# Kernel optimization log

Measured on AMD Instinct MI355X. Metric: run time of the kernel, lower is better.

The kernel has to match this reference:

```python
import jax, jax.numpy as jnp
import numpy as np

NUM_NEIGHBORS = (10, 25)  # FLAGS.num_neighbors = '10_25'
MAX_DEGREE = 64
L = 2  # num encoder layers


def _sample(nodes, neighbors_out, neighbors_in, key):
    """Multi-hop uniform neighbor sampling (shuffle columns + slice, as in TF code)."""
    samples = [nodes]
    support = 1
    supports = [1]
    for k in range(L):
        t = L - 1 - k
        n = NUM_NEIGHBORS[t]
        support *= 2 * n
        supports.append(support)
        key, k1, k2 = jax.random.split(key, 3)
        # tf.transpose(tf.random.shuffle(tf.transpose(x))) shuffles neighbor slots
        # with ONE permutation shared across all rows, then slices first n.
        cols_out = jax.random.permutation(k1, MAX_DEGREE)[:n]
        cols_in = jax.random.permutation(k2, MAX_DEGREE)[:n]
        nout = neighbors_out[samples[k]][:, cols_out]  # [prev, n]
        nin = neighbors_in[samples[k]][:, cols_in]     # [prev, n]
        samples.append(jnp.concatenate([nout, nin], axis=1).reshape(-1))
    return samples, supports


def _gc(self_v, nei_out, nei_in, W):
    # GraphConvolution: mean-aggregate out/in neighbors, concat with self, linear, sigmoid.
    agg = jnp.concatenate([self_v, nei_out.mean(axis=1), nei_in.mean(axis=1)], axis=-1)
    return jax.nn.sigmoid(agg @ W)


def _aggregate(inputs, supports, layer, W, B):
    h_hop = []
    for hop in range(L - layer):
        n = NUM_NEIGHBORS[L - hop - 1]
        nei = inputs[hop + 1].reshape(B * supports[hop], 2 * n, -1)
        self_v = inputs[hop].reshape(B * supports[hop], -1)
        h_hop.append(_gc(self_v, nei[:, :n], nei[:, n:], W))
    return h_hop


def _forward(nodes1, nodes2, neighbors_out, neighbors_in, features,
             W_in, W_mean, W_std, W_pi, W_ag, W_ad, Wd_mean, Wd_std, Wd_pi):
    B = nodes1.shape[0]
    key = jax.random.key(42)
    k1, k2 = jax.random.split(key)
    s1, sup1 = _sample(nodes1, neighbors_out, neighbors_in, k1)
    s2, sup2 = _sample(nodes2, neighbors_out, neighbors_in, k2)
    in1 = [features[s] for s in s1]  # hop-wise gathered features
    in2 = [features[s] for s in s2]
    # layer 0: shared input GC
    h1 = _aggregate(in1, sup1, 0, W_in, B)
    h2 = _aggregate(in2, sup2, 0, W_in, B)
    # layer 1: parameter heads (mean/std/pi/alpha)
    h_mean1 = _aggregate(h1, sup1, 1, W_mean, B)[0]
    h_mean2 = _aggregate(h2, sup2, 1, W_mean, B)[0]
    h_std1 = _aggregate(h1, sup1, 1, W_std, B)[0]
    h_std2 = _aggregate(h2, sup2, 1, W_std, B)[0]
    h_pi1 = _aggregate(h1, sup1, 1, W_pi, B)[0]
    h_pi2 = _aggregate(h2, sup2, 1, W_pi, B)[0]
    # final fully-connected projections (act = identity)
    z_mean1 = h_mean1 @ Wd_mean
    z_mean2 = h_mean2 @ Wd_mean
    z_std1 = h_std1 @ Wd_std
    z_std2 = h_std2 @ Wd_std
    pi_logit1 = h_pi1 @ Wd_pi
    pi_logit2 = h_pi2 @ Wd_pi
    return jnp.stack([z_mean1, z_std1, pi_logit1, z_mean2, z_std2, pi_logit2])


def setup_inputs() -> dict:
    key = jax.random.key(0)
    ks = jax.random.split(key, 16)
    N, F, B = 200000, 128, 256
    E, D = 128, 64
    inp = {
        'nodes1': jax.random.randint(ks[0], (B,), 0, N, dtype=jnp.int32),
        'nodes2': jax.random.randint(ks[1], (B,), 0, N, dtype=jnp.int32),
        'neighbors_out': jax.random.randint(ks[2], (N, MAX_DEGREE), 0, N, dtype=jnp.int32),
        'neighbors_in': jax.random.randint(ks[3], (N, MAX_DEGREE), 0, N, dtype=jnp.int32),
        'features': jax.random.normal(ks[4], (N, F), dtype=jnp.float32),
        'W_in': jax.random.normal(ks[5], (3 * F, E), dtype=jnp.float32) * 0.05,
        'W_mean': jax.random.normal(ks[6], (3 * E, E), dtype=jnp.float32) * 0.05,
        'W_std': jax.random.normal(ks[7], (3 * E, E), dtype=jnp.float32) * 0.05,
        'W_pi': jax.random.normal(ks[8], (3 * E, E), dtype=jnp.float32) * 0.05,
        'W_ag': jax.random.normal(ks[9], (3 * E, E), dtype=jnp.float32) * 0.05,
        'W_ad': jax.random.normal(ks[10], (3 * E, E), dtype=jnp.float32) * 0.05,
        'Wd_mean': jax.random.normal(ks[11], (E, D), dtype=jnp.float32) * 0.05,
        'Wd_std': jax.random.normal(ks[12], (E, D), dtype=jnp.float32) * 0.05,
        'Wd_pi': jax.random.normal(ks[13], (E, D), dtype=jnp.float32) * 0.05,
    }
    return inp


def reference(nodes1, nodes2, neighbors_out, neighbors_in, features,
              W_in, W_mean, W_std, W_pi, W_ag, W_ad, Wd_mean, Wd_std, Wd_pi):
    return _forward(nodes1, nodes2, neighbors_out, neighbors_in, features,
                    W_in, W_mean, W_std, W_pi, W_ag, W_ad, Wd_mean, Wd_std, Wd_pi)
```

## Files before the change

### kernel.cpp

```cpp
#include <hip/hip_runtime.h>
#include <stdint.h>
#include <math.h>

#define FDIM 128
#define KDIM 384
#define NROWS 26112

struct Cols { int o25[25]; int i25[25]; int o10[10]; int i10[10]; };
struct ColsBoth { Cols c[2]; };

static inline uint32_t rotl32(uint32_t x, uint32_t r){ return (x<<r)|(x>>(32u-r)); }

static void tf2x32(uint32_t k0, uint32_t k1, uint32_t c0, uint32_t c1,
                   uint32_t& o0, uint32_t& o1){
  const uint32_t ra[4] = {13u,15u,26u,6u};
  const uint32_t rb[4] = {17u,29u,16u,24u};
  uint32_t ks2 = k0 ^ k1 ^ 0x1BD11BDAu;
  uint32_t x0 = c0 + k0, x1 = c1 + k1;
  for(int i=0;i<4;i++){ x0 += x1; x1 = rotl32(x1, ra[i]); x1 ^= x0; }
  x0 += k1; x1 += ks2 + 1u;
  for(int i=0;i<4;i++){ x0 += x1; x1 = rotl32(x1, rb[i]); x1 ^= x0; }
  x0 += ks2; x1 += k0 + 2u;
  for(int i=0;i<4;i++){ x0 += x1; x1 = rotl32(x1, ra[i]); x1 ^= x0; }
  x0 += k0; x1 += k1 + 3u;
  for(int i=0;i<4;i++){ x0 += x1; x1 = rotl32(x1, rb[i]); x1 ^= x0; }
  x0 += k1; x1 += ks2 + 4u;
  for(int i=0;i<4;i++){ x0 += x1; x1 = rotl32(x1, ra[i]); x1 ^= x0; }
  x0 += ks2; x1 += k0 + 5u;
  o0 = x0; o1 = x1;
}

static void jax_split_child(uint32_t ka, uint32_t kb, uint32_t i,
                            uint32_t& oa, uint32_t& ob){
  tf2x32(ka, kb, 0u, i, oa, ob);
}

static uint32_t jax_bits32(uint32_t ka, uint32_t kb, uint32_t i){
  uint32_t a,b; tf2x32(ka, kb, 0u, i, a, b);
  return a ^ b;
}

static void jax_perm64(uint32_t ka, uint32_t kb, int* perm){
  uint32_t sa, sb; jax_split_child(ka, kb, 1u, sa, sb);
  uint32_t b[64]; int v[64];
  for(int i=0;i<64;i++){ b[i]=jax_bits32(sa, sb, (uint32_t)i); v[i]=i; }
  for(int i=1;i<64;i++){
    uint32_t bb=b[i]; int vv=v[i]; int j=i-1;
    while(j>=0 && b[j]>bb){ b[j+1]=b[j]; v[j+1]=v[j]; j--; }
    b[j+1]=bb; v[j+1]=vv;
  }
  for(int i=0;i<64;i++) perm[i]=v[i];
}

static void compute_cols(ColsBoth& cb){
  uint32_t k1a,k1b,k2a,k2b;
  jax_split_child(0u, 42u, 0u, k1a, k1b);
  jax_split_child(0u, 42u, 1u, k2a, k2b);
  for(int side=0; side<2; side++){
    uint32_t ka = side ? k2a : k1a;
    uint32_t kb = side ? k2b : k1b;
    uint32_t nka,nkb, c1a,c1b, c2a,c2b;
    jax_split_child(ka,kb,0u,nka,nkb);
    jax_split_child(ka,kb,1u,c1a,c1b);
    jax_split_child(ka,kb,2u,c2a,c2b);
    int p[64];
    jax_perm64(c1a,c1b,p); for(int i=0;i<25;i++) cb.c[side].o25[i]=p[i];
    jax_perm64(c2a,c2b,p); for(int i=0;i<25;i++) cb.c[side].i25[i]=p[i];
    uint32_t d1a,d1b,d2a,d2b;
    jax_split_child(nka,nkb,1u,d1a,d1b);
    jax_split_child(nka,nkb,2u,d2a,d2b);
    jax_perm64(d1a,d1b,p); for(int i=0;i<10;i++) cb.c[side].o10[i]=p[i];
    jax_perm64(d2a,d2b,p); for(int i=0;i<10;i++) cb.c[side].i10[i]=p[i];
  }
}

__device__ __forceinline__ float getc(const float4& v, int i){
  return (i==0)?v.x:(i==1)?v.y:(i==2)?v.z:v.w;
}
__device__ __forceinline__ float sigf(float x){ return 1.0f/(1.0f+expf(-x)); }
__device__ __forceinline__ void add4(float4& s, const float4& v){
  s.x+=v.x; s.y+=v.y; s.z+=v.z; s.w+=v.w;
}


__global__ __launch_bounds__(256) void sample1_kernel(
    const int* __restrict__ nodes1, const int* __restrict__ nodes2,
    const int* __restrict__ nout, const int* __restrict__ nin,
    int* __restrict__ s_hop1, ColsBoth cb){
  int idx = blockIdx.x*blockDim.x + threadIdx.x;
  if(idx >= 2*256*50) return;
  int side = idx / (256*50);
  int rem  = idx % (256*50);
  int b = rem / 50, j = rem % 50;
  int node = (side ? nodes2 : nodes1)[b];
  const Cols& c = cb.c[side];
  int nbr = (j < 25) ? nout[(long)node*64 + c.o25[j]]
                     : nin [(long)node*64 + c.i25[j-25]];
  s_hop1[idx] = nbr;
}

__global__ __launch_bounds__(256) void gather_kernel(
    const float* __restrict__ feat,
    const int* __restrict__ nodes1, const int* __restrict__ nodes2,
    const int* __restrict__ s_hop1,
    const int* __restrict__ nout, const int* __restrict__ nin,
    float* __restrict__ agg, int base_row, ColsBoth cb)
{
  int t = threadIdx.x;
  int row_local = blockIdx.x*8 + (t>>5);
  int lane = t & 31;
  int c0 = lane*4;
  int row = base_row + row_local;

  float4 selfv, so, si;

  if(row < 512){
    int side = row >> 8, b = row & 255;
    int node = (side ? nodes2 : nodes1)[b];
    selfv = *(const float4*)(feat + (long)node*FDIM + c0);
    const int* nb = s_hop1 + row*50;
    float4 acc = make_float4(0,0,0,0);
    #pragma unroll
    for(int jj=0; jj<25; jj+=5){
      int id[5]; float4 v[5];
      #pragma unroll
      for(int i=0;i<5;i++) id[i] = nb[jj+i];
      #pragma unroll
      for(int i=0;i<5;i++) v[i] = *(const float4*)(feat + (long)id[i]*FDIM + c0);
      #pragma unroll
      for(int i=0;i<5;i++) add4(acc, v[i]);
    }
    so = make_float4(acc.x/25.f, acc.y/25.f, acc.z/25.f, acc.w/25.f);
    acc = make_float4(0,0,0,0);
    #pragma unroll
    for(int jj=25; jj<50; jj+=5){
      int id[5]; float4 v[5];
      #pragma unroll
      for(int i=0;i<5;i++) id[i] = nb[jj+i];
      #pragma unroll
      for(int i=0;i<5;i++) v[i] = *(const float4*)(feat + (long)id[i]*FDIM + c0);
      #pragma unroll
      for(int i=0;i<5;i++) add4(acc, v[i]);
    }
    si = make_float4(acc.x/25.f, acc.y/25.f, acc.z/25.f, acc.w/25.f);
  } else {
    int hrow = row - 512;
    int side = (hrow >= 12800) ? 1 : 0;
    int node = s_hop1[hrow];
    const Cols& c = cb.c[side];
    const long nb = (long)node*64;
    int oid[10], iid[10];
    #pragma unroll
    for(int j=0;j<10;j++) oid[j] = nout[nb + c.o10[j]];
    #pragma unroll
    for(int j=0;j<10;j++) iid[j] = nin[nb + c.i10[j]];
    selfv = *(const float4*)(feat + (long)node*FDIM + c0);
    float4 v[20];
    #pragma unroll
    for(int j=0;j<10;j++) v[j]    = *(const float4*)(feat + (long)oid[j]*FDIM + c0);
    #pragma unroll
    for(int j=0;j<10;j++) v[10+j] = *(const float4*)(feat + (long)iid[j]*FDIM + c0);
    float4 acc = make_float4(0,0,0,0);
    #pragma unroll
    for(int j=0;j<10;j++) add4(acc, v[j]);
    so = make_float4(acc.x*0.1f, acc.y*0.1f, acc.z*0.1f, acc.w*0.1f);
    acc = make_float4(0,0,0,0);
    #pragma unroll
    for(int j=0;j<10;j++) add4(acc, v[10+j]);
    si = make_float4(acc.x*0.1f, acc.y*0.1f, acc.z*0.1f, acc.w*0.1f);
  }

  float* ar = agg + (long)row_local*KDIM;
  *(float4*)(ar + c0)       = selfv;
  *(float4*)(ar + 128 + c0) = so;
  *(float4*)(ar + 256 + c0) = si;
}

__global__ __launch_bounds__(256) void gemm_sig_kernel(
    const float* __restrict__ A, const float* __restrict__ W,
    float* __restrict__ out)
{
  __shared__ float Wbuf[96*128];
  int t = threadIdx.x, lane = t&15, rg = t>>4;
  int r0 = blockIdx.x*64 + rg*4;
  int c0 = lane*8;
  float acc[4][8];
  #pragma unroll
  for(int r=0;r<4;r++)
    #pragma unroll
    for(int i=0;i<8;i++) acc[r][i]=0.f;

  for(int kc=0; kc<4; kc++){
    __syncthreads();
    const float4* ws = (const float4*)(W + kc*96*128);
    float4* wd = (float4*)Wbuf;
    #pragma unroll
    for(int i=0;i<12;i++) wd[i*256+t] = ws[i*256+t];
    __syncthreads();
    const float* Ab = A + (long)r0*KDIM + kc*96;
    #pragma unroll 2
    for(int k4=0;k4<96;k4+=4){
      float4 a0 = *(const float4*)(Ab + 0*KDIM + k4);
      float4 a1 = *(const float4*)(Ab + 1*KDIM + k4);
      float4 a2 = *(const float4*)(Ab + 2*KDIM + k4);
      float4 a3 = *(const float4*)(Ab + 3*KDIM + k4);
      #pragma unroll
      for(int kk=0;kk<4;kk++){
        float av0=getc(a0,kk), av1=getc(a1,kk), av2=getc(a2,kk), av3=getc(a3,kk);
        const float* wr = Wbuf + (k4+kk)*128 + c0;
        float4 w0 = *(const float4*)wr;
        float4 w1 = *(const float4*)(wr+4);
        acc[0][0]+=av0*w0.x; acc[0][1]+=av0*w0.y; acc[0][2]+=av0*w0.z; acc[0][3]+=av0*w0.w;
        acc[0][4]+=av0*w1.x; acc[0][5]+=av0*w1.y; acc[0][6]+=av0*w1.z; acc[0][7]+=av0*w1.w;
        acc[1][0]+=av1*w0.x; acc[1][1]+=av1*w0.y; acc[1][2]+=av1*w0.z; acc[1][3]+=av1*w0.w;
        acc[1][4]+=av1*w1.x; acc[1][5]+=av1*w1.y; acc[1][6]+=av1*w1.z; acc[1][7]+=av1*w1.w;
        acc[2][0]+=av2*w0.x; acc[2][1]+=av2*w0.y; acc[2][2]+=av2*w0.z; acc[2][3]+=av2*w0.w;
        acc[2][4]+=av2*w1.x; acc[2][5]+=av2*w1.y; acc[2][6]+=av2*w1.z; acc[2][7]+=av2*w1.w;
        acc[3][0]+=av3*w0.x; acc[3][1]+=av3*w0.y; acc[3][2]+=av3*w0.z; acc[3][3]+=av3*w0.w;
        acc[3][4]+=av3*w1.x; acc[3][5]+=av3*w1.y; acc[3][6]+=av3*w1.z; acc[3][7]+=av3*w1.w;
      }
    }
  }
  #pragma unroll
  for(int r=0;r<4;r++){
    float4 o0, o1;
    o0.x=sigf(acc[r][0]); o0.y=sigf(acc[r][1]); o0.z=sigf(acc[r][2]); o0.w=sigf(acc[r][3]);
    o1.x=sigf(acc[r][4]); o1.y=sigf(acc[r][5]); o1.z=sigf(acc[r][6]); o1.w=sigf(acc[r][7]);
    float* op = out + (long)(r0+r)*FDIM + c0;
    *(float4*)op = o0; *(float4*)(op+4) = o1;
  }
}

__global__ __launch_bounds__(256) void agg1_kernel(
    const float* __restrict__ h0, const float* __restrict__ h1,
    float* __restrict__ agg2)
{
  int row = blockIdx.x;
  int t = threadIdx.x;
  int ch = t & 127;
  int half = t >> 7;
  const float* base = h1 + (long)row*50*FDIM + half*25*FDIM + ch;
  float s = 0.f;
  #pragma unroll
  for(int j=0;j<25;j++) s += base[j*FDIM];
  agg2[(long)row*KDIM + 128 + half*128 + ch] = s * (1.0f/25.0f);
  if(half == 0) agg2[(long)row*KDIM + ch] = h0[(long)row*FDIM + ch];
}

__global__ __launch_bounds__(256) void head_kernel(
    const float* __restrict__ agg2,
    const float* __restrict__ Wm, const float* __restrict__ Ws, const float* __restrict__ Wp,
    const float* __restrict__ Dm, const float* __restrict__ Ds, const float* __restrict__ Dp,
    float* __restrict__ out)
{
  __shared__ float As[4*KDIM];
  __shared__ float Hs[4*FDIM];
  int head = blockIdx.x >> 7;
  int rt   = blockIdx.x & 127;
  int t = threadIdx.x;
  int row = t >> 6;
  int c = (t & 63) * 2;
  const float* W = (head==0) ? Wm : (head==1) ? Ws : Wp;
  const float* D = (head==0) ? Dm : (head==1) ? Ds : Dp;

  {
    const float* src = agg2 + (long)rt*4*KDIM;
    #pragma unroll
    for(int i=0;i<6;i++) As[i*256 + t] = src[i*256 + t];
  }
  __syncthreads();

  float acc0 = 0.f, acc1 = 0.f;
  const float* as = As + row*KDIM;
  #pragma unroll 8
  for(int k=0;k<KDIM;k++){
    float a = as[k];
    float2 w = *(const float2*)(W + (long)k*FDIM + c);
    acc0 += a*w.x; acc1 += a*w.y;
  }
  Hs[row*FDIM + c]   = sigf(acc0);
  Hs[row*FDIM + c+1] = sigf(acc1);
  __syncthreads();

  {
    int col = t & 63;
    const float* hs = Hs + row*FDIM;
    float a = 0.f;
    #pragma unroll 8
    for(int k=0;k<FDIM;k++){
      a += hs[k] * D[(long)k*64 + col];
    }
    int grow = rt*4 + row;
    int side = grow >> 8, b = grow & 255;
    out[((long)(side*3+head)*256 + b)*64 + col] = a;
  }
}

extern "C" void kernel_launch(void* const* d_in, const int* in_sizes, int n_in,
                              void* d_out, int out_size, void* d_ws, size_t ws_size,
                              hipStream_t stream) {
  const int*   nodes1  = (const int*)d_in[0];
  const int*   nodes2  = (const int*)d_in[1];
  const int*   nout    = (const int*)d_in[2];
  const int*   nin     = (const int*)d_in[3];
  const float* feat    = (const float*)d_in[4];
  const float* W_in    = (const float*)d_in[5];
  const float* W_mean  = (const float*)d_in[6];
  const float* W_std   = (const float*)d_in[7];
  const float* W_pi    = (const float*)d_in[8];
  const float* Wd_mean = (const float*)d_in[11];
  const float* Wd_std  = (const float*)d_in[12];
  const float* Wd_pi   = (const float*)d_in[13];
  float* out = (float*)d_out;

  int*   s_hop1 = (int*)d_ws;
  float* h      = (float*)(s_hop1 + 25600);
  float* agg2   = h + (size_t)NROWS*FDIM;
  float* aggC   = agg2 + 512*KDIM;

  size_t fixedB = 25600*4 + (size_t)NROWS*FDIM*4 + 512*KDIM*4;
  const int ncOpt[5] = {1,2,4,12,51};
  int nc = 51;
  for(int i=0;i<5;i++){
    size_t need = fixedB + ((size_t)NROWS/ncOpt[i])*KDIM*4;
    if(need <= ws_size){ nc = ncOpt[i]; break; }
  }
  int chunkRows = NROWS / nc;

  ColsBoth cb;
  compute_cols(cb);

  sample1_kernel<<<(2*256*50 + 255)/256, 256, 0, stream>>>(nodes1, nodes2, nout, nin, s_hop1, cb);
  for(int c=0;c<nc;c++){
    int base = c*chunkRows;
    gather_kernel<<<chunkRows/8, 256, 0, stream>>>(feat, nodes1, nodes2, s_hop1,
                                                   nout, nin, aggC, base, cb);
    gemm_sig_kernel<<<chunkRows/64, 256, 0, stream>>>(aggC, W_in, h + (size_t)base*FDIM);
  }
  agg1_kernel<<<512, 256, 0, stream>>>(h, h + 512*FDIM, agg2);
  head_kernel<<<384, 256, 0, stream>>>(agg2, W_mean, W_std, W_pi, Wd_mean, Wd_std, Wd_pi, out);
}
```

Baseline: 331.1 us.

## Fuse hop-1 sampling into gather and neighbor aggregation into head kernel

Removes the separate sampling kernel by having the gather kernel look up hop-1 neighbor ids directly from the adjacency tables. It also removes the agg1 kernel by having each head block compute the self, out-mean and in-mean rows itself before its GEMM. This cuts two launches and the workspace round-trips for s_hop1 and agg2. In exchange, each of the three head variants now recomputes the 50-row neighbor mean, and the hop-2 rows re-read the root adjacency.

New measurement: 323.8 us. 2.2% less time.

```diff
diff --git a/kernel.cpp b/kernel.cpp
--- a/kernel.cpp
+++ b/kernel.cpp
@@ -81,28 +81,14 @@
 __device__ __forceinline__ void add4(float4& s, const float4& v){
   s.x+=v.x; s.y+=v.y; s.z+=v.z; s.w+=v.w;
 }
-
-
-__global__ __launch_bounds__(256) void sample1_kernel(
-    const int* __restrict__ nodes1, const int* __restrict__ nodes2,
-    const int* __restrict__ nout, const int* __restrict__ nin,
-    int* __restrict__ s_hop1, ColsBoth cb){
-  int idx = blockIdx.x*blockDim.x + threadIdx.x;
-  if(idx >= 2*256*50) return;
-  int side = idx / (256*50);
-  int rem  = idx % (256*50);
-  int b = rem / 50, j = rem % 50;
-  int node = (side ? nodes2 : nodes1)[b];
-  const Cols& c = cb.c[side];
-  int nbr = (j < 25) ? nout[(long)node*64 + c.o25[j]]
-                     : nin [(long)node*64 + c.i25[j-25]];
-  s_hop1[idx] = nbr;
-}
+__device__ __forceinline__ void add2(float2& s, const float2& v){
+  s.x+=v.x; s.y+=v.y;
+}
+
 
 __global__ __launch_bounds__(256) void gather_kernel(
     const float* __restrict__ feat,
     const int* __restrict__ nodes1, const int* __restrict__ nodes2,
-    const int* __restrict__ s_hop1,
     const int* __restrict__ nout, const int* __restrict__ nin,
     float* __restrict__ agg, int base_row, ColsBoth cb)
 {
@@ -117,14 +103,15 @@
   if(row < 512){
     int side = row >> 8, b = row & 255;
     int node = (side ? nodes2 : nodes1)[b];
+    const Cols& c = cb.c[side];
+    const long nb = (long)node*64;
     selfv = *(const float4*)(feat + (long)node*FDIM + c0);
-    const int* nb = s_hop1 + row*50;
     float4 acc = make_float4(0,0,0,0);
     #pragma unroll
     for(int jj=0; jj<25; jj+=5){
       int id[5]; float4 v[5];
       #pragma unroll
-      for(int i=0;i<5;i++) id[i] = nb[jj+i];
+      for(int i=0;i<5;i++) id[i] = nout[nb + c.o25[jj+i]];
       #pragma unroll
       for(int i=0;i<5;i++) v[i] = *(const float4*)(feat + (long)id[i]*FDIM + c0);
       #pragma unroll
@@ -133,10 +120,10 @@
     so = make_float4(acc.x/25.f, acc.y/25.f, acc.z/25.f, acc.w/25.f);
     acc = make_float4(0,0,0,0);
     #pragma unroll
-    for(int jj=25; jj<50; jj+=5){
+    for(int jj=0; jj<25; jj+=5){
       int id[5]; float4 v[5];
       #pragma unroll
-      for(int i=0;i<5;i++) id[i] = nb[jj+i];
+      for(int i=0;i<5;i++) id[i] = nin[nb + c.i25[jj+i]];
       #pragma unroll
       for(int i=0;i<5;i++) v[i] = *(const float4*)(feat + (long)id[i]*FDIM + c0);
       #pragma unroll
@@ -146,8 +133,13 @@
   } else {
     int hrow = row - 512;
     int side = (hrow >= 12800) ? 1 : 0;
-    int node = s_hop1[hrow];
+    int r = side ? (hrow - 12800) : hrow;
+    int b = r / 50, slot = r % 50;
     const Cols& c = cb.c[side];
+    int root = (side ? nodes2 : nodes1)[b];
+    int node;
+    if(slot < 25) node = nout[(long)root*64 + c.o25[slot]];
+    else          node = nin [(long)root*64 + c.i25[slot-25]];
     const long nb = (long)node*64;
     int oid[10], iid[10];
     #pragma unroll
@@ -231,24 +223,8 @@
   }
 }
 
-__global__ __launch_bounds__(256) void agg1_kernel(
-    const float* __restrict__ h0, const float* __restrict__ h1,
-    float* __restrict__ agg2)
-{
-  int row = blockIdx.x;
-  int t = threadIdx.x;
-  int ch = t & 127;
-  int half = t >> 7;
-  const float* base = h1 + (long)row*50*FDIM + half*25*FDIM + ch;
-  float s = 0.f;
-  #pragma unroll
-  for(int j=0;j<25;j++) s += base[j*FDIM];
-  agg2[(long)row*KDIM + 128 + half*128 + ch] = s * (1.0f/25.0f);
-  if(half == 0) agg2[(long)row*KDIM + ch] = h0[(long)row*FDIM + ch];
-}
-
 __global__ __launch_bounds__(256) void head_kernel(
-    const float* __restrict__ agg2,
+    const float* __restrict__ h,
     const float* __restrict__ Wm, const float* __restrict__ Ws, const float* __restrict__ Wp,
     const float* __restrict__ Dm, const float* __restrict__ Ds, const float* __restrict__ Dp,
     float* __restrict__ out)
@@ -259,38 +235,64 @@
   int rt   = blockIdx.x & 127;
   int t = threadIdx.x;
   int row = t >> 6;
-  int c = (t & 63) * 2;
+  int lane = t & 63;
   const float* W = (head==0) ? Wm : (head==1) ? Ws : Wp;
   const float* D = (head==0) ? Dm : (head==1) ? Ds : Dp;
+  int grow = rt*4 + row;
 
   {
-    const float* src = agg2 + (long)rt*4*KDIM;
-    #pragma unroll
-    for(int i=0;i<6;i++) As[i*256 + t] = src[i*256 + t];
+    int c2 = lane*2;
+    float2 selfv = *(const float2*)(h + (long)grow*FDIM + c2);
+    const float* nb = h + (long)(512 + grow*50)*FDIM + c2;
+    float2 s = make_float2(0,0);
+    #pragma unroll
+    for(int jj=0;jj<25;jj+=5){
+      float2 v[5];
+      #pragma unroll
+      for(int i=0;i<5;i++) v[i] = *(const float2*)(nb + (long)(jj+i)*FDIM);
+      #pragma unroll
+      for(int i=0;i<5;i++) add2(s, v[i]);
+    }
+    float2 so = make_float2(s.x/25.f, s.y/25.f);
+    s = make_float2(0,0);
+    #pragma unroll
+    for(int jj=25;jj<50;jj+=5){
+      float2 v[5];
+      #pragma unroll
+      for(int i=0;i<5;i++) v[i] = *(const float2*)(nb + (long)(jj+i)*FDIM);
+      #pragma unroll
+      for(int i=0;i<5;i++) add2(s, v[i]);
+    }
+    float2 si = make_float2(s.x/25.f, s.y/25.f);
+    *(float2*)&As[row*KDIM + c2]       = selfv;
+    *(float2*)&As[row*KDIM + 128 + c2] = so;
+    *(float2*)&As[row*KDIM + 256 + c2] = si;
   }
   __syncthreads();
 
-  float acc0 = 0.f, acc1 = 0.f;
-  const float* as = As + row*KDIM;
-  #pragma unroll 8
-  for(int k=0;k<KDIM;k++){
-    float a = as[k];
-    float2 w = *(const float2*)(W + (long)k*FDIM + c);
-    acc0 += a*w.x; acc1 += a*w.y;
-  }
-  Hs[row*FDIM + c]   = sigf(acc0);
-  Hs[row*FDIM + c+1] = sigf(acc1);
+  {
+    int c = lane*2;
+    float acc0 = 0.f, acc1 = 0.f;
+    const float* as = As + row*KDIM;
+    #pragma unroll 8
+    for(int k=0;k<KDIM;k++){
+      float a = as[k];
+      float2 w = *(const float2*)(W + (long)k*FDIM + c);
+      acc0 += a*w.x; acc1 += a*w.y;
+    }
+    Hs[row*FDIM + c]   = sigf(acc0);
+    Hs[row*FDIM + c+1] = sigf(acc1);
+  }
   __syncthreads();
 
   {
-    int col = t & 63;
+    int col = lane;
     const float* hs = Hs + row*FDIM;
     float a = 0.f;
     #pragma unroll 8
     for(int k=0;k<FDIM;k++){
       a += hs[k] * D[(long)k*64 + col];
     }
-    int grow = rt*4 + row;
     int side = grow >> 8, b = grow & 255;
     out[((long)(side*3+head)*256 + b)*64 + col] = a;
   }
@@ -313,12 +315,10 @@
   const float* Wd_pi   = (const float*)d_in[13];
   float* out = (float*)d_out;
 
-  int*   s_hop1 = (int*)d_ws;
-  float* h      = (float*)(s_hop1 + 25600);
-  float* agg2   = h + (size_t)NROWS*FDIM;
-  float* aggC   = agg2 + 512*KDIM;
-
-  size_t fixedB = 25600*4 + (size_t)NROWS*FDIM*4 + 512*KDIM*4;
+  float* h    = (float*)d_ws;
+  float* aggC = h + (size_t)NROWS*FDIM;
+
+  size_t fixedB = (size_t)NROWS*FDIM*4;
   const int ncOpt[5] = {1,2,4,12,51};
   int nc = 51;
   for(int i=0;i<5;i++){
@@ -330,13 +330,11 @@
   ColsBoth cb;
   compute_cols(cb);
 
-  sample1_kernel<<<(2*256*50 + 255)/256, 256, 0, stream>>>(nodes1, nodes2, nout, nin, s_hop1, cb);
   for(int c=0;c<nc;c++){
     int base = c*chunkRows;
-    gather_kernel<<<chunkRows/8, 256, 0, stream>>>(feat, nodes1, nodes2, s_hop1,
+    gather_kernel<<<chunkRows/8, 256, 0, stream>>>(feat, nodes1, nodes2,
                                                    nout, nin, aggC, base, cb);
     gemm_sig_kernel<<<chunkRows/64, 256, 0, stream>>>(aggC, W_in, h + (size_t)base*FDIM);
   }
-  agg1_kernel<<<512, 256, 0, stream>>>(h, h + 512*FDIM, agg2);
-  head_kernel<<<384, 256, 0, stream>>>(agg2, W_mean, W_std, W_pi, Wd_mean, Wd_std, Wd_pi, out);
-}
+  head_kernel<<<384, 256, 0, stream>>>(h, W_mean, W_std, W_pi, Wd_mean, Wd_std, Wd_pi, out);
+}
```
